# Kernel optimization log

Hardware: AMD Instinct MI355X
Metric: run time of the kernel (lower is better)

The kernel has to match this reference:

```python
import jax, jax.numpy as jnp
import numpy as np

D = 1024       # hidden_dim
H = 16         # n_heads
HD = D // H    # head dim = 64
V = 32000      # vocab_size
S = 4          # n_scales
IT = 6         # iters_per_scale
L = S * IT     # total_layers = 24 (one shared block, looped)
G = 16         # n_rot_groups
g = D // G     # group dim = 64
FF = 4 * D     # ff_mult * hidden_dim
N_TRI = g * (g - 1) // 2  # 2016 upper-tri skew params per group
EPS = 1e-6


def rmsnorm(x, w):
    return x * jax.lax.rsqrt(jnp.mean(x * x, axis=-1, keepdims=True) + EPS) * w


def setup_inputs() -> dict:
    key = jax.random.key(0)
    ks = jax.random.split(key, 12)
    rn = lambda k, shape, s: jax.random.normal(k, shape, jnp.float32) * s
    return {
        "tokens": jax.random.randint(ks[0], (1, 1024), 0, V),
        "embed_w": rn(ks[1], (V, D), 0.02),
        "lm_head_w": rn(ks[2], (V, D), 0.02),
        "norm_w": jnp.ones((D,), jnp.float32),
        "layer_gamma": 1.0 + rn(ks[3], (L, D), 0.02),
        "layer_beta": rn(ks[4], (L, D), 0.02),
        "iter_scale": 1.0 + rn(ks[5], (S, IT), 0.02),
        "skew_upper": rn(ks[6], (L, G, N_TRI), 0.02),
        "ln1_w": jnp.ones((D,), jnp.float32),
        "ln2_w": jnp.ones((D,), jnp.float32),
        "wqkv": rn(ks[7], (D, 3 * D), 0.02),
        "wo": rn(ks[8], (D, D), 0.02),
        "w1": rn(ks[9], (D, FF), 0.02),
        "w2": rn(ks[10], (FF, D), 0.02),
    }


def _rotations(skew_upper):
    """Cayley transform per layer/group: R = (I - A/2)^-1 (I + A/2), A skew-symm."""
    rows, cols = np.triu_indices(g, k=1)
    def one_layer(su):  # su: (G, N_TRI)
        A = jnp.zeros((G, g, g), su.dtype).at[:, rows, cols].set(su)
        A = A - jnp.swapaxes(A, -1, -2)
        I = jnp.eye(g, dtype=su.dtype)
        return jnp.linalg.solve(I - 0.5 * A, I + 0.5 * A)  # (G, g, g)
    return jax.vmap(one_layer)(skew_upper)  # (L, G, g, g)


def _block(x, gamma, beta, ln1_w, ln2_w, wqkv, wo, w1, w2):
    """Pre-norm causal transformer block with (gamma, beta) affine modulation."""
    B, T, _ = x.shape
    h = rmsnorm(x, ln1_w) * gamma + beta
    qkv = h @ wqkv  # (B, T, 3D)
    q, k, v = jnp.split(qkv, 3, axis=-1)
    q = q.reshape(B, T, H, HD)
    k = k.reshape(B, T, H, HD)
    v = v.reshape(B, T, H, HD)
    scores = jnp.einsum('bqhd,bkhd->bhqk', q, k) / np.sqrt(HD).astype(np.float32)
    causal = jnp.tril(jnp.ones((T, T), bool))
    scores = jnp.where(causal, scores, jnp.float32(-1e9))
    attn = jax.nn.softmax(scores, axis=-1)
    attn_out = jnp.einsum('bhqk,bkhd->bqhd', attn, v).reshape(B, T, D) @ wo
    x = x + attn_out
    x = x + jax.nn.gelu(rmsnorm(x, ln2_w) @ w1) @ w2
    return x


def reference(tokens, embed_w, lm_head_w, norm_w, layer_gamma, layer_beta,
              iter_scale, skew_upper, ln1_w, ln2_w, wqkv, wo, w1, w2):
    B, T = tokens.shape
    x = embed_w[tokens].astype(jnp.float32)  # (B, T, D)
    R = _rotations(skew_upper)               # (L, G, g, g)
    its = iter_scale.reshape(-1)             # (L,) scale index order matches loop
    for l in range(L):
        blk = _block(x, layer_gamma[l], layer_beta[l], ln1_w, ln2_w, wqkv, wo, w1, w2)
        x = x + (blk - x) * its[l]           # affine residual blend
        xg = x.reshape(B, T, G, g)
        x = jnp.einsum('btgi,gij->btgj', xg, R[l]).reshape(B, T, D)  # group rotation
    x = rmsnorm(x, norm_w)
    return x @ lm_head_w.T                   # (B, T, V) logits
```

## Files before the change

kernel.cpp:

```cpp
#include <hip/hip_runtime.h>
#include <hip/hip_bf16.h>
#include <math.h>

constexpr int kD = 1024;
constexpr int kH = 16;
constexpr int kV = 32000;
constexpr int kT = 1024;
constexpr int kG = 16;
constexpr int kFF = 4096;
constexpr int kL = 24;
constexpr int kNTRI = 2016;
#define EPSF 1e-6f
#define L2E 1.44269504088896f

typedef __bf16 bf16x8 __attribute__((ext_vector_type(8)));
typedef __bf16 bf16x4 __attribute__((ext_vector_type(4)));
typedef float f32x4 __attribute__((ext_vector_type(4)));

#define GLOAD16(g, l)                                                   \
  __builtin_amdgcn_global_load_lds(                                     \
      (const __attribute__((address_space(1))) void*)(g),               \
      (__attribute__((address_space(3))) void*)(l), 16, 0, 0)

__global__ __launch_bounds__(256) void cayley_kernel(const float* __restrict__ skew,
                                                     float* __restrict__ R) {
  int lg = blockIdx.x;
  int tid = threadIdx.x;
  int r = tid & 63, q = tid >> 6;
  __shared__ float Ms[64][65];
  __shared__ float Bs[64][65];
  const float* su = skew + (size_t)lg * kNTRI;
#pragma unroll
  for (int cc = 0; cc < 16; ++cc) {
    int c = q * 16 + cc;
    float a = 0.f;
    if (r < c) a = su[r * (127 - r) / 2 + (c - r - 1)];
    else if (r > c) a = -su[c * (127 - c) / 2 + (r - c - 1)];
    Ms[r][c] = (r == c ? 1.f : 0.f) - 0.5f * a;
    Bs[r][c] = (r == c ? 1.f : 0.f) + 0.5f * a;
  }
  __syncthreads();
  for (int k = 0; k < 64; ++k) {
    float ip = 1.f / Ms[k][k];
    float f = Ms[r][k];
    float beta = (r == k) ? (1.f - ip) : (f * ip);
    float mk[16], bk[16];
#pragma unroll
    for (int cc = 0; cc < 16; ++cc) {
      mk[cc] = Ms[k][q * 16 + cc];
      bk[cc] = Bs[k][q * 16 + cc];
    }
    __syncthreads();
#pragma unroll
    for (int cc = 0; cc < 16; ++cc) {
      int c = q * 16 + cc;
      Ms[r][c] -= beta * mk[cc];
      Bs[r][c] -= beta * bk[cc];
    }
    __syncthreads();
  }
  float* Ro = R + ((size_t)lg * 64 + r) * 64;
#pragma unroll
  for (int cc = 0; cc < 16; ++cc) Ro[q * 16 + cc] = Bs[r][q * 16 + cc];
}

__global__ __launch_bounds__(256) void embed_kernel(const int* __restrict__ tok,
                                                    const float* __restrict__ ew,
                                                    float* __restrict__ x) {
  int i = blockIdx.x * 256 + threadIdx.x;
  int t = i >> 8;
  int d4 = i & 255;
  int v = tok[t];
  reinterpret_cast<float4*>(x)[i] =
      reinterpret_cast<const float4*>(ew + (size_t)v * kD)[d4];
}

__global__ __launch_bounds__(256) void cast_kernel(const float* __restrict__ W,
                                                   __bf16* __restrict__ O) {
  size_t i = ((size_t)blockIdx.x * 256 + threadIdx.x) * 8;
  float4 f0 = *reinterpret_cast<const float4*>(W + i);
  float4 f1 = *reinterpret_cast<const float4*>(W + i + 4);
  bf16x8 v;
  v[0] = (__bf16)f0.x; v[1] = (__bf16)f0.y;
  v[2] = (__bf16)f0.z; v[3] = (__bf16)f0.w;
  v[4] = (__bf16)f1.x; v[5] = (__bf16)f1.y;
  v[6] = (__bf16)f1.z; v[7] = (__bf16)f1.w;
  *reinterpret_cast<bf16x8*>(O + i) = v;
}

__global__ __launch_bounds__(256) void convt_kernel(const float* __restrict__ W,
                                                    __bf16* __restrict__ WT,
                                                    int K, int N) {
  __shared__ float tile[64][65];
  int t = threadIdx.x;
  int n0 = blockIdx.x * 64, k0 = blockIdx.y * 64;
#pragma unroll
  for (int r = 0; r < 4; ++r) {
    int kr = r * 16 + (t >> 4);
    int nc = (t & 15) * 4;
    float4 v = *reinterpret_cast<const float4*>(&W[(size_t)(k0 + kr) * N + n0 + nc]);
    tile[kr][nc + 0] = v.x;
    tile[kr][nc + 1] = v.y;
    tile[kr][nc + 2] = v.z;
    tile[kr][nc + 3] = v.w;
  }
  __syncthreads();
#pragma unroll
  for (int r = 0; r < 2; ++r) {
    int idx = r * 256 + t;
    int nrow = idx >> 3, kc = (idx & 7) * 8;
    bf16x8 v;
#pragma unroll
    for (int j = 0; j < 8; ++j) v[j] = (__bf16)tile[kc + j][nrow];
    *reinterpret_cast<bf16x8*>(&WT[(size_t)(n0 + nrow) * K + k0 + kc]) = v;
  }
}

template <bool AFFINE>
__global__ __launch_bounds__(256) void rms_kernel(const float* __restrict__ x,
                                                  const float* __restrict__ w,
                                                  const float* __restrict__ gamma,
                                                  const float* __restrict__ beta,
                                                  __bf16* __restrict__ out) {
  int t = blockIdx.x, tid = threadIdx.x;
  __shared__ float red4[4];
  float4 xv = reinterpret_cast<const float4*>(x + (size_t)t * kD)[tid];
  float ss = xv.x * xv.x + xv.y * xv.y + xv.z * xv.z + xv.w * xv.w;
#pragma unroll
  for (int o = 1; o < 64; o <<= 1) ss += __shfl_xor(ss, o);
  if ((tid & 63) == 0) red4[tid >> 6] = ss;
  __syncthreads();
  float tot = red4[0] + red4[1] + red4[2] + red4[3];
  float rms = rsqrtf(tot / (float)kD + EPSF);
  float4 wv = reinterpret_cast<const float4*>(w)[tid];
  float o0 = xv.x * rms * wv.x;
  float o1 = xv.y * rms * wv.y;
  float o2 = xv.z * rms * wv.z;
  float o3 = xv.w * rms * wv.w;
  if (AFFINE) {
    float4 gv = reinterpret_cast<const float4*>(gamma)[tid];
    float4 bv = reinterpret_cast<const float4*>(beta)[tid];
    o0 = o0 * gv.x + bv.x;
    o1 = o1 * gv.y + bv.y;
    o2 = o2 * gv.z + bv.z;
    o3 = o3 * gv.w + bv.w;
  }
  bf16x4 ov;
  ov[0] = (__bf16)o0; ov[1] = (__bf16)o1; ov[2] = (__bf16)o2; ov[3] = (__bf16)o3;
  *reinterpret_cast<bf16x4*>(out + (size_t)t * kD + tid * 4) = ov;
}

template <int BM, int BN, int NW, int EPI, bool BF32>
__global__ __launch_bounds__(NW * 64) void gemm_kernel(
    const __bf16* __restrict__ A, const void* __restrict__ Bv,
    const float* res, void* __restrict__ Cv, int M, int N, int K) {
  constexpr int WCOLS = (NW == 4) ? 2 : 4;
  constexpr int FM = (BM / 2) / 16;
  constexpr int FN = (BN / WCOLS) / 16;
  constexpr int AISS = BM / 8 / NW;
  constexpr int BISS = BN / 8 / NW;
  __shared__ __bf16 As[BM * 64];
  __shared__ __bf16 Bs[BN * 64];
  char* AsB = (char*)As;
  char* BsB = (char*)Bs;
  int tid = threadIdx.x;
  int w = tid >> 6, lane = tid & 63;
  int mt = M / BM;
  int cpx = gridDim.x >> 3;
  int id = (blockIdx.x & 7) * cpx + (blockIdx.x >> 3);
  int bm = (id % mt) * BM, bn = (id / mt) * BN;
  int lrow = lane & 15, g = lane >> 4;
  int grow = lane >> 3;
  int gswz = ((lane & 7) ^ grow) * 8;
  int rsw = (lrow & 7) << 4;
  int wm = (NW == 4) ? (w >> 1) : (w >> 2);
  int wn = (NW == 4) ? (w & 1) : (w & 3);
  int wr = wm * (BM / 2), wc = wn * (BN / WCOLS);
  f32x4 acc[FM][FN] = {};
  const __bf16* B16 = (const __bf16*)Bv;
  const float* B32 = (const float*)Bv;

  for (int k0 = 0; k0 < K; k0 += 64) {
#pragma unroll
    for (int i = 0; i < AISS; ++i) {
      int rbase = (i * NW + w) * 8;
      GLOAD16(&A[(size_t)(bm + rbase + grow) * K + k0 + gswz], &As[rbase * 64]);
    }
    if (!BF32) {
#pragma unroll
      for (int i = 0; i < BISS; ++i) {
        int rbase = (i * NW + w) * 8;
        GLOAD16(&B16[(size_t)(bn + rbase + grow) * K + k0 + gswz], &Bs[rbase * 64]);
      }
    } else {
#pragma unroll
      for (int rrep = 0; rrep < BN * 8 / (NW * 64); ++rrep) {
        int cid = rrep * NW * 64 + tid;
        int row = cid >> 3, kc = (cid & 7) * 8;
        const float* src = &B32[(size_t)(bn + row) * K + k0 + kc];
        float4 f0 = *reinterpret_cast<const float4*>(src);
        float4 f1 = *reinterpret_cast<const float4*>(src + 4);
        bf16x8 v;
        v[0] = (__bf16)f0.x; v[1] = (__bf16)f0.y;
        v[2] = (__bf16)f0.z; v[3] = (__bf16)f0.w;
        v[4] = (__bf16)f1.x; v[5] = (__bf16)f1.y;
        v[6] = (__bf16)f1.z; v[7] = (__bf16)f1.w;
        int swc = ((cid & 7) ^ (row & 7)) * 16;
        *reinterpret_cast<bf16x8*>(BsB + row * 128 + swc) = v;
      }
    }
    __syncthreads();
#pragma unroll
    for (int ks = 0; ks < 2; ++ks) {
      bf16x8 af[FM], bg[FN];
#pragma unroll
      for (int i = 0; i < FM; ++i)
        af[i] = *reinterpret_cast<const bf16x8*>(
            AsB + (wr + i * 16 + lrow) * 128 + ((ks * 64 + g * 16) ^ rsw));
#pragma unroll
      for (int j = 0; j < FN; ++j)
        bg[j] = *reinterpret_cast<const bf16x8*>(
            BsB + (wc + j * 16 + lrow) * 128 + ((ks * 64 + g * 16) ^ rsw));
#pragma unroll
      for (int i = 0; i < FM; ++i)
#pragma unroll
        for (int j = 0; j < FN; ++j)
          acc[i][j] = __builtin_amdgcn_mfma_f32_16x16x32_bf16(af[i], bg[j],
                                                              acc[i][j], 0, 0, 0);
    }
    __syncthreads();
  }

  int crow0 = bm + wr + g * 4;
  int ccol0 = bn + wc + lrow;
#pragma unroll
  for (int i = 0; i < FM; ++i) {
#pragma unroll
    for (int j = 0; j < FN; ++j) {
#pragma unroll
      for (int r = 0; r < 4; ++r) {
        int row = crow0 + i * 16 + r;
        int col = ccol0 + j * 16;
        size_t idx = (size_t)row * N + col;
        float v = acc[i][j][r];
        if (EPI == 1) v += res[idx];
        if (EPI == 2) {
          float u = v;
          float z = 0.7978845608028654f * (u + 0.044715f * u * u * u);
          float ez = exp2f(z * (2.f * L2E));
          v = u * ez / (1.f + ez);
        }
        if (EPI == 2 || EPI == 3) ((__bf16*)Cv)[idx] = (__bf16)v;
        else ((float*)Cv)[idx] = v;
      }
    }
  }
}

__global__ __launch_bounds__(256) void fattn_kernel(const __bf16* __restrict__ qkv,
                                                    __bf16* __restrict__ out) {
  __shared__ __bf16 Ks[2][64 * 64];
  __shared__ __bf16 Vt[2][64 * 64];
  __shared__ __bf16 Ps[4 * 16 * 64];
  int tid = threadIdx.x;
  int bq = blockIdx.x * 64;
  int h = blockIdx.y;
  int w = tid >> 6, lane = tid & 63;
  int g = lane >> 4, lr = lane & 15;

  bf16x8 qf[2];
  const __bf16* qbase = qkv + (size_t)(bq + w * 16 + lr) * (3 * kD) + h * 64;
#pragma unroll
  for (int ks = 0; ks < 2; ++ks) {
    bf16x8 v = *reinterpret_cast<const bf16x8*>(qbase + ks * 32 + g * 8);
#pragma unroll
    for (int j = 0; j < 8; ++j) qf[ks][j] = (__bf16)((float)v[j] * 0.125f);
  }

  f32x4 acc[4] = {};
  float m = -1e30f, lsum = 0.f;

  int srow = tid >> 2, sseg = tid & 3;
  int vk = tid & 63, vd0 = (tid >> 6) * 16;
  char* PwB = (char*)(Ps + w * (16 * 64));
  int psw = (lr & 7) << 4;

  bf16x8 ka, kb2, va, vb;
  int ntiles = bq / 64 + 1;

  {
    const __bf16* src = qkv + (size_t)(srow) * (3 * kD) + kD + h * 64 + sseg * 16;
    ka = *reinterpret_cast<const bf16x8*>(src);
    kb2 = *reinterpret_cast<const bf16x8*>(src + 8);
    const __bf16* vsrc = qkv + (size_t)(vk) * (3 * kD) + 2 * kD + h * 64 + vd0;
    va = *reinterpret_cast<const bf16x8*>(vsrc);
    vb = *reinterpret_cast<const bf16x8*>(vsrc + 8);
    char* KsB = (char*)Ks[0];
    char* VtB = (char*)Vt[0];
    int bc = sseg * 32, sw = (srow & 7) << 4;
    *reinterpret_cast<bf16x8*>(KsB + srow * 128 + (bc ^ sw)) = ka;
    *reinterpret_cast<bf16x8*>(KsB + srow * 128 + ((bc + 16) ^ sw)) = kb2;
#pragma unroll
    for (int i = 0; i < 8; ++i) {
      int d = vd0 + i;
      *((__bf16*)(VtB + d * 128 + ((vk * 2) ^ ((d & 7) << 4)))) = va[i];
      d = vd0 + 8 + i;
      *((__bf16*)(VtB + d * 128 + ((vk * 2) ^ ((d & 7) << 4)))) = vb[i];
    }
  }

  int cur = 0;
  for (int kt = 0; kt < ntiles; ++kt) {
    if (kt + 1 < ntiles) {
      const __bf16* src =
          qkv + (size_t)((kt + 1) * 64 + srow) * (3 * kD) + kD + h * 64 + sseg * 16;
      ka = *reinterpret_cast<const bf16x8*>(src);
      kb2 = *reinterpret_cast<const bf16x8*>(src + 8);
      const __bf16* vsrc =
          qkv + (size_t)((kt + 1) * 64 + vk) * (3 * kD) + 2 * kD + h * 64 + vd0;
      va = *reinterpret_cast<const bf16x8*>(vsrc);
      vb = *reinterpret_cast<const bf16x8*>(vsrc + 8);
    }
    __syncthreads();

    char* KsB = (char*)Ks[cur];
    char* VtB = (char*)Vt[cur];
    bool diag = (kt == ntiles - 1);
    int jmax = diag ? w : 3;

    f32x4 s[4];
#pragma unroll
    for (int jj = 0; jj < 4; ++jj) {
      if (jj <= jmax) {
        int krow = jj * 16 + lr;
        int ksw = (lr & 7) << 4;
        bf16x8 k0 = *reinterpret_cast<const bf16x8*>(KsB + krow * 128 + ((g * 16) ^ ksw));
        bf16x8 k1 = *reinterpret_cast<const bf16x8*>(KsB + krow * 128 + ((64 + g * 16) ^ ksw));
        f32x4 z = {};
        z = __builtin_amdgcn_mfma_f32_16x16x32_bf16(k0, qf[0], z, 0, 0, 0);
        s[jj] = __builtin_amdgcn_mfma_f32_16x16x32_bf16(k1, qf[1], z, 0, 0, 0);
      } else {
        s[jj] = f32x4{-1e30f, -1e30f, -1e30f, -1e30f};
      }
    }
    if (diag) {
#pragma unroll
      for (int r = 0; r < 4; ++r)
        if (g * 4 + r > lr) s[w][r] = -1e30f;
    }

    float mt = -1e30f;
#pragma unroll
    for (int jj = 0; jj < 4; ++jj)
#pragma unroll
      for (int r = 0; r < 4; ++r) mt = fmaxf(mt, s[jj][r]);
    mt = fmaxf(mt, __shfl_xor(mt, 16));
    mt = fmaxf(mt, __shfl_xor(mt, 32));
    float mn = fmaxf(m, mt);
    float sc = exp2f((m - mn) * L2E);
    float p[4][4];
    float rs = 0.f;
#pragma unroll
    for (int jj = 0; jj < 4; ++jj)
#pragma unroll
      for (int r = 0; r < 4; ++r) {
        float e = exp2f((s[jj][r] - mn) * L2E);
        p[jj][r] = e;
        rs += e;
      }
    rs += __shfl_xor(rs, 16);
    rs += __shfl_xor(rs, 32);
    lsum = lsum * sc + rs;
    m = mn;
#pragma unroll
    for (int r = 0; r < 4; ++r) {
      float s4 = __shfl(sc, 20 * g + r);
#pragma unroll
      for (int dt = 0; dt < 4; ++dt) acc[dt][r] *= s4;
    }

#pragma unroll
    for (int jj = 0; jj < 4; ++jj) {
      bf16x4 pv;
#pragma unroll
      for (int r = 0; r < 4; ++r) pv[r] = (__bf16)p[jj][r];
      *reinterpret_cast<bf16x4*>(PwB + lr * 128 + ((jj * 32 + g * 8) ^ psw)) = pv;
    }

    {
      bf16x8 pa0 = *reinterpret_cast<const bf16x8*>(PwB + lr * 128 + ((g * 16) ^ psw));
      bf16x8 pa1 = *reinterpret_cast<const bf16x8*>(PwB + lr * 128 + ((64 + g * 16) ^ psw));
#pragma unroll
      for (int dt = 0; dt < 4; ++dt) {
        int vrow = dt * 16 + lr;
        int vsw = (lr & 7) << 4;
        bf16x8 vb0 = *reinterpret_cast<const bf16x8*>(VtB + vrow * 128 + ((g * 16) ^ vsw));
        bf16x8 vb1 = *reinterpret_cast<const bf16x8*>(VtB + vrow * 128 + ((64 + g * 16) ^ vsw));
        acc[dt] = __builtin_amdgcn_mfma_f32_16x16x32_bf16(pa0, vb0, acc[dt], 0, 0, 0);
        acc[dt] = __builtin_amdgcn_mfma_f32_16x16x32_bf16(pa1, vb1, acc[dt], 0, 0, 0);
      }
    }
    __syncthreads();

    if (kt + 1 < ntiles) {
      char* KsN = (char*)Ks[cur ^ 1];
      char* VtN = (char*)Vt[cur ^ 1];
      int bc = sseg * 32, sw = (srow & 7) << 4;
      *reinterpret_cast<bf16x8*>(KsN + srow * 128 + (bc ^ sw)) = ka;
      *reinterpret_cast<bf16x8*>(KsN + srow * 128 + ((bc + 16) ^ sw)) = kb2;
#pragma unroll
      for (int i = 0; i < 8; ++i) {
        int d = vd0 + i;
        *((__bf16*)(VtN + d * 128 + ((vk * 2) ^ ((d & 7) << 4)))) = va[i];
        d = vd0 + 8 + i;
        *((__bf16*)(VtN + d * 128 + ((vk * 2) ^ ((d & 7) << 4)))) = vb[i];
      }
      cur ^= 1;
    }
  }

  float linv = 1.f / lsum;
#pragma unroll
  for (int r = 0; r < 4; ++r) {
    float ir = __shfl(linv, 20 * g + r);
    int row = bq + w * 16 + g * 4 + r;
#pragma unroll
    for (int dt = 0; dt < 4; ++dt)
      out[(size_t)row * kD + h * 64 + dt * 16 + lr] = (__bf16)(acc[dt][r] * ir);
  }
}

__global__ __launch_bounds__(256) void blend_rot_kernel(const float* x,
                                                        const float* y,
                                                        const float* iscale,
                                                        int l,
                                                        const float* __restrict__ Rall,
                                                        float* xout) {
  int tc = blockIdx.x, gr = blockIdx.y;
  int tid = threadIdx.x;
  __shared__ float Rs[64 * 64];
  __shared__ float xb[64][65];
  float s = iscale[l];
  const float* Rg = Rall + ((size_t)l * kG + gr) * 4096;
  {
    int off = tid * 16;
#pragma unroll
    for (int q2 = 0; q2 < 4; ++q2) {
      float4 rv = *reinterpret_cast<const float4*>(Rg + off + q2 * 4);
      *reinterpret_cast<float4*>(&Rs[off + q2 * 4]) = rv;
    }
  }
  int tok = tid & 63, seg = (tid >> 6) * 16;
  {
    const float* xr = x + (size_t)(tc * 64 + tok) * kD + gr * 64 + seg;
    const float* yr = y + (size_t)(tc * 64 + tok) * kD + gr * 64 + seg;
#pragma unroll
    for (int q2 = 0; q2 < 4; ++q2) {
      float4 xv = *reinterpret_cast<const float4*>(xr + q2 * 4);
      float4 yv = *reinterpret_cast<const float4*>(yr + q2 * 4);
      xb[tok][seg + q2 * 4 + 0] = xv.x + (yv.x - xv.x) * s;
      xb[tok][seg + q2 * 4 + 1] = xv.y + (yv.y - xv.y) * s;
      xb[tok][seg + q2 * 4 + 2] = xv.z + (yv.z - xv.z) * s;
      xb[tok][seg + q2 * 4 + 3] = xv.w + (yv.w - xv.w) * s;
    }
  }
  __syncthreads();
  float o[16] = {};
  for (int i = 0; i < 64; ++i) {
    float xv = xb[tok][i];
#pragma unroll
    for (int d = 0; d < 16; ++d) o[d] += xv * Rs[i * 64 + seg + d];
  }
  float* outr = xout + (size_t)(tc * 64 + tok) * kD + gr * 64 + seg;
#pragma unroll
  for (int q2 = 0; q2 < 4; ++q2) {
    float4 ov = {o[q2 * 4 + 0], o[q2 * 4 + 1], o[q2 * 4 + 2], o[q2 * 4 + 3]};
    *reinterpret_cast<float4*>(outr + q2 * 4) = ov;
  }
}

extern "C" void kernel_launch(void* const* d_in, const int* in_sizes, int n_in,
                              void* d_out, int out_size, void* d_ws, size_t ws_size,
                              hipStream_t stream) {
  const int* tokens = (const int*)d_in[0];
  const float* embed_w = (const float*)d_in[1];
  const float* lm_head_w = (const float*)d_in[2];
  const float* norm_w = (const float*)d_in[3];
  const float* layer_gamma = (const float*)d_in[4];
  const float* layer_beta = (const float*)d_in[5];
  const float* iter_scale = (const float*)d_in[6];
  const float* skew_upper = (const float*)d_in[7];
  const float* ln1_w = (const float*)d_in[8];
  const float* ln2_w = (const float*)d_in[9];
  const float* wqkv = (const float*)d_in[10];
  const float* wo = (const float*)d_in[11];
  const float* w1 = (const float*)d_in[12];
  const float* w2 = (const float*)d_in[13];
  float* out = (float*)d_out;

  float* x = (float*)d_ws;
  float* y = x + (size_t)kT * kD;
  __bf16* hb = (__bf16*)(y + (size_t)kT * kD);
  __bf16* ab = hb + (size_t)kT * kD;
  float* R = (float*)(ab + (size_t)kT * kD);
  __bf16* lmhb = (__bf16*)(R + (size_t)kL * kG * 4096);
  bool ws_big = ws_size >= (size_t)(4670464 + 16384000) * 4;

  __bf16* qkvb = (__bf16*)out;
  __bf16* ffb = (__bf16*)(out + 1572864);
  __bf16* wqkvT = (__bf16*)(out + 3670016);
  __bf16* woT = (__bf16*)(out + 5242880);
  __bf16* w1T = (__bf16*)(out + 5767168);
  __bf16* w2T = (__bf16*)(out + 7864320);

  cayley_kernel<<<kL * kG, 256, 0, stream>>>(skew_upper, R);
  embed_kernel<<<kT * kD / 4 / 256, 256, 0, stream>>>(tokens, embed_w, x);
  convt_kernel<<<dim3(3 * kD / 64, kD / 64), 256, 0, stream>>>(wqkv, wqkvT, kD, 3 * kD);
  convt_kernel<<<dim3(kD / 64, kD / 64), 256, 0, stream>>>(wo, woT, kD, kD);
  convt_kernel<<<dim3(kFF / 64, kD / 64), 256, 0, stream>>>(w1, w1T, kD, kFF);
  convt_kernel<<<dim3(kD / 64, kFF / 64), 256, 0, stream>>>(w2, w2T, kFF, kD);
  if (ws_big)
    cast_kernel<<<kV * kD / 8 / 256, 256, 0, stream>>>(lm_head_w, lmhb);

  for (int l = 0; l < kL; ++l) {
    rms_kernel<true><<<kT, 256, 0, stream>>>(x, ln1_w, layer_gamma + (size_t)l * kD,
                                             layer_beta + (size_t)l * kD, hb);
    gemm_kernel<64, 128, 8, 3, false><<<(kT / 64) * (3 * kD / 128), 512, 0, stream>>>(
        hb, wqkvT, nullptr, qkvb, kT, 3 * kD, kD);
    fattn_kernel<<<dim3(kT / 64, kH), 256, 0, stream>>>(qkvb, ab);
    gemm_kernel<64, 64, 8, 1, false><<<(kT / 64) * (kD / 64), 512, 0, stream>>>(
        ab, woT, x, y, kT, kD, kD);
    rms_kernel<false><<<kT, 256, 0, stream>>>(y, ln2_w, nullptr, nullptr, hb);
    gemm_kernel<64, 128, 8, 2, false><<<(kT / 64) * (kFF / 128), 512, 0, stream>>>(
        hb, w1T, nullptr, ffb, kT, kFF, kD);
    gemm_kernel<64, 64, 8, 1, false><<<(kT / 64) * (kD / 64), 512, 0, stream>>>(
        ffb, w2T, y, y, kT, kD, kFF);
    blend_rot_kernel<<<dim3(kT / 64, kG), 256, 0, stream>>>(x, y, iter_scale, l, R, x);
  }

  rms_kernel<false><<<kT, 256, 0, stream>>>(x, norm_w, nullptr, nullptr, hb);
  if (ws_big)
    gemm_kernel<128, 128, 4, 0, false><<<(kT / 128) * (kV / 128), 256, 0, stream>>>(
        hb, lmhb, nullptr, out, kT, kV, kD);
  else
    gemm_kernel<128, 128, 4, 0, true><<<(kT / 128) * (kV / 128), 256, 0, stream>>>(
        hb, lm_head_w, nullptr, out, kT, kV, kD);
}
```

Baseline: 3.088 ms.

## Split-K the wo and w2 GEMMs and fold partial sums into rmsnorm and blend

The two N=1024 GEMMs (wo and w2) now run split-K by 2, doubling the block count from 256 to 512 to fill more CUs. Each half writes an fp32 partial buffer. The partials and the residual are summed inside a new fused residual+rmsnorm kernel and inside the blend/rotation kernel. The LM-head GEMM also moves to 256x128 tiles with 8 waves. This trades extra partial-buffer global traffic for better occupancy on the small GEMMs.

Result: faster. 2.651 ms (-14.2%).

```diff
diff --git a/kernel.cpp b/kernel.cpp
--- a/kernel.cpp
+++ b/kernel.cpp
@@ -150,7 +150,41 @@
   *reinterpret_cast<bf16x4*>(out + (size_t)t * kD + tid * 4) = ov;
 }
 
-template <int BM, int BN, int NW, int EPI, bool BF32>
+__global__ __launch_bounds__(256) void rms_red_kernel(const float* __restrict__ x,
+                                                      const float* __restrict__ p0,
+                                                      const float* __restrict__ p1,
+                                                      const float* __restrict__ w,
+                                                      float* __restrict__ y,
+                                                      __bf16* __restrict__ hb) {
+  int t = blockIdx.x, tid = threadIdx.x;
+  __shared__ float red4[4];
+  size_t base = (size_t)t * kD;
+  float4 xv = reinterpret_cast<const float4*>(x + base)[tid];
+  float4 a = reinterpret_cast<const float4*>(p0 + base)[tid];
+  float4 b = reinterpret_cast<const float4*>(p1 + base)[tid];
+  float4 yv;
+  yv.x = xv.x + a.x + b.x;
+  yv.y = xv.y + a.y + b.y;
+  yv.z = xv.z + a.z + b.z;
+  yv.w = xv.w + a.w + b.w;
+  reinterpret_cast<float4*>(y + base)[tid] = yv;
+  float ss = yv.x * yv.x + yv.y * yv.y + yv.z * yv.z + yv.w * yv.w;
+#pragma unroll
+  for (int o = 1; o < 64; o <<= 1) ss += __shfl_xor(ss, o);
+  if ((tid & 63) == 0) red4[tid >> 6] = ss;
+  __syncthreads();
+  float tot = red4[0] + red4[1] + red4[2] + red4[3];
+  float rms = rsqrtf(tot / (float)kD + EPSF);
+  float4 wv = reinterpret_cast<const float4*>(w)[tid];
+  bf16x4 ov;
+  ov[0] = (__bf16)(yv.x * rms * wv.x);
+  ov[1] = (__bf16)(yv.y * rms * wv.y);
+  ov[2] = (__bf16)(yv.z * rms * wv.z);
+  ov[3] = (__bf16)(yv.w * rms * wv.w);
+  *reinterpret_cast<bf16x4*>(hb + base + tid * 4) = ov;
+}
+
+template <int BM, int BN, int NW, int EPI, bool BF32, int KSPLIT = 1>
 __global__ __launch_bounds__(NW * 64) void gemm_kernel(
     const __bf16* __restrict__ A, const void* __restrict__ Bv,
     const float* res, void* __restrict__ Cv, int M, int N, int K) {
@@ -165,10 +199,13 @@
   char* BsB = (char*)Bs;
   int tid = threadIdx.x;
   int w = tid >> 6, lane = tid & 63;
-  int mt = M / BM;
+  int mt = M / BM, nt = N / BN;
   int cpx = gridDim.x >> 3;
   int id = (blockIdx.x & 7) * cpx + (blockIdx.x >> 3);
-  int bm = (id % mt) * BM, bn = (id / mt) * BN;
+  int ks_id = id / (mt * nt);
+  int rem = id % (mt * nt);
+  int bm = (rem % mt) * BM, bn = (rem / mt) * BN;
+  int kbeg = ks_id * (K / KSPLIT), kend = kbeg + K / KSPLIT;
   int lrow = lane & 15, g = lane >> 4;
   int grow = lane >> 3;
   int gswz = ((lane & 7) ^ grow) * 8;
@@ -180,7 +217,7 @@
   const __bf16* B16 = (const __bf16*)Bv;
   const float* B32 = (const float*)Bv;
 
-  for (int k0 = 0; k0 < K; k0 += 64) {
+  for (int k0 = kbeg; k0 < kend; k0 += 64) {
 #pragma unroll
     for (int i = 0; i < AISS; ++i) {
       int rbase = (i * NW + w) * 8;
@@ -231,6 +268,7 @@
     __syncthreads();
   }
 
+  float* Cp = (float*)Cv + (size_t)ks_id * M * N;
   int crow0 = bm + wr + g * 4;
   int ccol0 = bn + wc + lrow;
 #pragma unroll
@@ -251,7 +289,7 @@
           v = u * ez / (1.f + ez);
         }
         if (EPI == 2 || EPI == 3) ((__bf16*)Cv)[idx] = (__bf16)v;
-        else ((float*)Cv)[idx] = v;
+        else Cp[idx] = v;
       }
     }
   }
@@ -432,6 +470,8 @@
 
 __global__ __launch_bounds__(256) void blend_rot_kernel(const float* x,
                                                         const float* y,
+                                                        const float* q0,
+                                                        const float* q1,
                                                         const float* iscale,
                                                         int l,
                                                         const float* __restrict__ Rall,
@@ -452,16 +492,21 @@
   }
   int tok = tid & 63, seg = (tid >> 6) * 16;
   {
-    const float* xr = x + (size_t)(tc * 64 + tok) * kD + gr * 64 + seg;
-    const float* yr = y + (size_t)(tc * 64 + tok) * kD + gr * 64 + seg;
+    size_t base = (size_t)(tc * 64 + tok) * kD + gr * 64 + seg;
 #pragma unroll
     for (int q2 = 0; q2 < 4; ++q2) {
-      float4 xv = *reinterpret_cast<const float4*>(xr + q2 * 4);
-      float4 yv = *reinterpret_cast<const float4*>(yr + q2 * 4);
-      xb[tok][seg + q2 * 4 + 0] = xv.x + (yv.x - xv.x) * s;
-      xb[tok][seg + q2 * 4 + 1] = xv.y + (yv.y - xv.y) * s;
-      xb[tok][seg + q2 * 4 + 2] = xv.z + (yv.z - xv.z) * s;
-      xb[tok][seg + q2 * 4 + 3] = xv.w + (yv.w - xv.w) * s;
+      float4 xv = *reinterpret_cast<const float4*>(x + base + q2 * 4);
+      float4 yv = *reinterpret_cast<const float4*>(y + base + q2 * 4);
+      float4 a = *reinterpret_cast<const float4*>(q0 + base + q2 * 4);
+      float4 b = *reinterpret_cast<const float4*>(q1 + base + q2 * 4);
+      float y0 = yv.x + a.x + b.x;
+      float y1 = yv.y + a.y + b.y;
+      float y2 = yv.z + a.z + b.z;
+      float y3 = yv.w + a.w + b.w;
+      xb[tok][seg + q2 * 4 + 0] = xv.x + (y0 - xv.x) * s;
+      xb[tok][seg + q2 * 4 + 1] = xv.y + (y1 - xv.y) * s;
+      xb[tok][seg + q2 * 4 + 2] = xv.z + (y2 - xv.z) * s;
+      xb[tok][seg + q2 * 4 + 3] = xv.w + (y3 - xv.w) * s;
     }
   }
   __syncthreads();
@@ -512,6 +557,8 @@
   __bf16* woT = (__bf16*)(out + 5242880);
   __bf16* w1T = (__bf16*)(out + 5767168);
   __bf16* w2T = (__bf16*)(out + 7864320);
+  float* wop = out + 9961472;
+  float* w2p = out + 12058624;
 
   cayley_kernel<<<kL * kG, 256, 0, stream>>>(skew_upper, R);
   embed_kernel<<<kT * kD / 4 / 256, 256, 0, stream>>>(tokens, embed_w, x);
@@ -528,19 +575,20 @@
     gemm_kernel<64, 128, 8, 3, false><<<(kT / 64) * (3 * kD / 128), 512, 0, stream>>>(
         hb, wqkvT, nullptr, qkvb, kT, 3 * kD, kD);
     fattn_kernel<<<dim3(kT / 64, kH), 256, 0, stream>>>(qkvb, ab);
-    gemm_kernel<64, 64, 8, 1, false><<<(kT / 64) * (kD / 64), 512, 0, stream>>>(
-        ab, woT, x, y, kT, kD, kD);
-    rms_kernel<false><<<kT, 256, 0, stream>>>(y, ln2_w, nullptr, nullptr, hb);
+    gemm_kernel<64, 64, 8, 0, false, 2><<<2 * (kT / 64) * (kD / 64), 512, 0, stream>>>(
+        ab, woT, nullptr, wop, kT, kD, kD);
+    rms_red_kernel<<<kT, 256, 0, stream>>>(x, wop, wop + (size_t)kT * kD, ln2_w, y, hb);
     gemm_kernel<64, 128, 8, 2, false><<<(kT / 64) * (kFF / 128), 512, 0, stream>>>(
         hb, w1T, nullptr, ffb, kT, kFF, kD);
-    gemm_kernel<64, 64, 8, 1, false><<<(kT / 64) * (kD / 64), 512, 0, stream>>>(
-        ffb, w2T, y, y, kT, kD, kFF);
-    blend_rot_kernel<<<dim3(kT / 64, kG), 256, 0, stream>>>(x, y, iter_scale, l, R, x);
+    gemm_kernel<64, 64, 8, 0, false, 2><<<2 * (kT / 64) * (kD / 64), 512, 0, stream>>>(
+        ffb, w2T, nullptr, w2p, kT, kD, kFF);
+    blend_rot_kernel<<<dim3(kT / 64, kG), 256, 0, stream>>>(
+        x, y, w2p, w2p + (size_t)kT * kD, iter_scale, l, R, x);
   }
 
   rms_kernel<false><<<kT, 256, 0, stream>>>(x, norm_w, nullptr, nullptr, hb);
   if (ws_big)
-    gemm_kernel<128, 128, 4, 0, false><<<(kT / 128) * (kV / 128), 256, 0, stream>>>(
+    gemm_kernel<256, 128, 8, 0, false><<<(kT / 256) * (kV / 128), 512, 0, stream>>>(
         hb, lmhb, nullptr, out, kT, kV, kD);
   else
     gemm_kernel<128, 128, 4, 0, true><<<(kT / 128) * (kV / 128), 256, 0, stream>>>(
```
